# Performance work log

Hardware: AMD Instinct MI355X
Metric: run time of the kernel (lower is better)

The kernel has to match this reference:

```python
import jax, jax.numpy as jnp
import numpy as np

B, S, D = 2, 2048, 1024
H = 16
DH = D // H


def _layernorm(x, g, b, eps=1e-5):
    mu = jnp.mean(x, axis=-1, keepdims=True)
    var = jnp.var(x, axis=-1, keepdims=True)
    return (x - mu) * jax.lax.rsqrt(var + eps) * g + b


def setup_inputs() -> dict:
    key = jax.random.key(0)
    ks = jax.random.split(key, 8)
    s = lambda fan_in: 1.0 / np.sqrt(fan_in)
    return {
        "x": jax.random.normal(ks[0], (B, S, D), dtype=jnp.float32),
        "ln1_g": jnp.ones((D,), jnp.float32),
        "ln1_b": jnp.zeros((D,), jnp.float32),
        "w_qkv": jax.random.uniform(ks[1], (D, 3 * D), jnp.float32, -s(D), s(D)),
        "b_qkv": jnp.zeros((3 * D,), jnp.float32),
        "w_out": jax.random.uniform(ks[2], (D, D), jnp.float32, -s(D), s(D)),
        "b_out": jnp.zeros((D,), jnp.float32),
        "ln2_g": jnp.ones((D,), jnp.float32),
        "ln2_b": jnp.zeros((D,), jnp.float32),
        "w1": jax.random.uniform(ks[3], (D, 4 * D), jnp.float32, -s(D), s(D)),
        "b1": jnp.zeros((4 * D,), jnp.float32),
        "w2": jax.random.uniform(ks[4], (4 * D, D), jnp.float32, -s(4 * D), s(4 * D)),
        "b2": jnp.zeros((D,), jnp.float32),
    }


def reference(x, ln1_g, ln1_b, w_qkv, b_qkv, w_out, b_out,
              ln2_g, ln2_b, w1, b1, w2, b2):
    scale = DH ** -0.5
    residual = x
    h = _layernorm(x, ln1_g, ln1_b)
    qkv = h @ w_qkv + b_qkv                      # [B,S,3D]
    q, k, v = jnp.split(qkv, 3, axis=-1)
    # [B,S,D] -> [B,H,S,DH]
    split_heads = lambda t: t.reshape(B, S, H, DH).transpose(0, 2, 1, 3)
    q, k, v = map(split_heads, (q, k, v))
    scores = jnp.einsum("bhsd,bhtd->bhst", q, k) * scale  # full O(S^2) matrix
    attn = jax.nn.softmax(scores, axis=-1)
    out = jnp.einsum("bhst,bhtd->bhsd", attn, v)
    out = out.transpose(0, 2, 1, 3).reshape(B, S, D)
    out = out @ w_out + b_out                    # dropout is identity at eval
    x = residual + out
    residual = x
    h = _layernorm(x, ln2_g, ln2_b)
    h = jax.nn.gelu(h @ w1 + b1, approximate=False)
    h = h @ w2 + b2
    return residual + h
```

## Files before the change

### kernel.cpp

```cpp
#include <hip/hip_runtime.h>
#include <hip/hip_bf16.h>
#include <math.h>

#define Bc 2
#define Sc 2048
#define Dc 1024
#define Hc 16
#define DHc 64
#define Mc (Bc*Sc)

typedef __attribute__((ext_vector_type(8))) short bf16x8;
typedef __attribute__((ext_vector_type(4))) float f32x4;
typedef __attribute__((ext_vector_type(16))) float f32x16;

#define QSCALE 0.18033688f

__device__ __forceinline__ ushort f2bf(float f){
  union { float f; uint32_t u; } c; c.f = f;
  uint32_t u = c.u;
  return (ushort)((u + 0x7fffu + ((u >> 16) & 1u)) >> 16);
}
__device__ __forceinline__ ushort f2bf_fast(float f){
  union { float f; uint32_t u; } c; c.f = f;
  return (ushort)((c.u + 0x8000u) >> 16);
}
__device__ __forceinline__ float fast_exp2(float x){
#if __has_builtin(__builtin_amdgcn_exp2f)
  return __builtin_amdgcn_exp2f(x);
#else
  return exp2f(x);
#endif
}

__device__ __forceinline__ void stage16(const void* g, void* lbase, int lane){
#if __has_builtin(__builtin_amdgcn_global_load_lds)
  __builtin_amdgcn_global_load_lds(
      (const __attribute__((address_space(1))) void*)g,
      (__attribute__((address_space(3))) void*)lbase, 16, 0, 0);
#else
  *(int4*)((char*)lbase + lane*16) = *(const int4*)g;
#endif
}

__global__ __launch_bounds__(256) void tcast(const float* __restrict__ w,
                                             ushort* __restrict__ wt,
                                             int K, int N){
  __shared__ float t[32][33];
  int kb = blockIdx.y * 32, nb = blockIdx.x * 32;
  int tx = threadIdx.x & 31, ty = threadIdx.x >> 5;
  #pragma unroll
  for (int i = 0; i < 4; i++)
    t[ty + 8*i][tx] = w[(size_t)(kb + ty + 8*i) * N + nb + tx];
  __syncthreads();
  #pragma unroll
  for (int i = 0; i < 4; i++)
    wt[(size_t)(nb + ty + 8*i) * K + kb + tx] = f2bf(t[tx][ty + 8*i]);
}

__global__ __launch_bounds__(256) void ln_bf16(const float* __restrict__ x,
                                               const float* __restrict__ g,
                                               const float* __restrict__ b,
                                               ushort* __restrict__ out){
  int row = blockIdx.x;
  const float4 xv = reinterpret_cast<const float4*>(x + (size_t)row * Dc)[threadIdx.x];
  float s  = xv.x + xv.y + xv.z + xv.w;
  float sq = xv.x*xv.x + xv.y*xv.y + xv.z*xv.z + xv.w*xv.w;
  #pragma unroll
  for (int m = 1; m < 64; m <<= 1){ s += __shfl_xor(s, m); sq += __shfl_xor(sq, m); }
  __shared__ float ss[4], ssq[4];
  int wv = threadIdx.x >> 6;
  if ((threadIdx.x & 63) == 0){ ss[wv] = s; ssq[wv] = sq; }
  __syncthreads();
  s  = ss[0] + ss[1] + ss[2] + ss[3];
  sq = ssq[0] + ssq[1] + ssq[2] + ssq[3];
  float mu  = s * (1.0f / Dc);
  float var = sq * (1.0f / Dc) - mu * mu;
  float rstd = rsqrtf(var + 1e-5f);
  float4 gv = reinterpret_cast<const float4*>(g)[threadIdx.x];
  float4 bv = reinterpret_cast<const float4*>(b)[threadIdx.x];
  ushort o[4];
  o[0] = f2bf((xv.x - mu) * rstd * gv.x + bv.x);
  o[1] = f2bf((xv.y - mu) * rstd * gv.y + bv.y);
  o[2] = f2bf((xv.z - mu) * rstd * gv.z + bv.z);
  o[3] = f2bf((xv.w - mu) * rstd * gv.w + bv.w);
  *reinterpret_cast<uint2*>(out + (size_t)row * Dc + threadIdx.x * 4) =
      *reinterpret_cast<uint2*>(o);
}

template<int EPI>
__global__ __launch_bounds__(256) void gemm128(
    const ushort* __restrict__ A, const ushort* __restrict__ BT,
    const float* __restrict__ bias,
    ushort* __restrict__ outb,
    ushort* __restrict__ oq, ushort* __restrict__ ok, ushort* __restrict__ ov,
    int N, int K){
  __shared__ short As[2][128*32];
  __shared__ short Bs[2][128*32];

  const int fid = blockIdx.x;
  const int q8 = gridDim.x >> 3;
  const int id2 = (fid & 7) * q8 + (fid >> 3);
  const int nbx = N / 128;
  const int nb = id2 % nbx, mb = id2 / nbx;

  const int tid = threadIdx.x;
  const int wave = tid >> 6, lane = tid & 63;
  const int wm = wave >> 1, wn = wave & 1;
  const int lr = lane & 15, lg = lane >> 4;

  f32x4 acc[4][4] = {};

  const int sr = tid >> 2;
  const int sc = ((tid & 3) * 8) ^ ((sr & 3) * 8);
  const ushort* Ag = A  + (size_t)(mb * 128 + sr) * K + sc;
  const ushort* Bg = BT + (size_t)(nb * 128 + sr) * K + sc;
  const int nK = K >> 5;

  {
    char* Ab = (char*)&As[0][0] + wave * 1024;
    char* Bb = (char*)&Bs[0][0] + wave * 1024;
    stage16(Ag,                 Ab,        lane);
    stage16(Ag + (size_t)64*K,  Ab + 4096, lane);
    stage16(Bg,                 Bb,        lane);
    stage16(Bg + (size_t)64*K,  Bb + 4096, lane);
  }
  __syncthreads();

  const int rsz = (lr & 3) * 8;

  for (int kt = 0; kt < nK; ++kt){
    const int cur = kt & 1;
    if (kt + 1 < nK){
      const int ko = (kt + 1) * 32;
      char* Ab = (char*)&As[cur ^ 1][0] + wave * 1024;
      char* Bb = (char*)&Bs[cur ^ 1][0] + wave * 1024;
      stage16(Ag + ko,                 Ab,        lane);
      stage16(Ag + (size_t)64*K + ko,  Ab + 4096, lane);
      stage16(Bg + ko,                 Bb,        lane);
      stage16(Bg + (size_t)64*K + ko,  Bb + 4096, lane);
    }
    bf16x8 af[4], bfr[4];
    #pragma unroll
    for (int mt = 0; mt < 4; mt++)
      af[mt] = *reinterpret_cast<const bf16x8*>(
          &As[cur][(wm*64 + mt*16 + lr)*32 + ((lg*8) ^ rsz)]);
    #pragma unroll
    for (int nt = 0; nt < 4; nt++)
      bfr[nt] = *reinterpret_cast<const bf16x8*>(
          &Bs[cur][(wn*64 + nt*16 + lr)*32 + ((lg*8) ^ rsz)]);
    #pragma unroll
    for (int mt = 0; mt < 4; mt++)
      #pragma unroll
      for (int nt = 0; nt < 4; nt++)
        acc[mt][nt] = __builtin_amdgcn_mfma_f32_16x16x32_bf16(af[mt], bfr[nt], acc[mt][nt], 0, 0, 0);
    __syncthreads();
  }

  if (EPI == 0){
    #pragma unroll
    for (int mt = 0; mt < 4; mt++){
      const int gm0 = mb * 128 + wm * 64 + mt * 16 + lg * 4;
      const int bb = gm0 >> 11, s0 = gm0 & 2047;
      #pragma unroll
      for (int nt = 0; nt < 4; nt++){
        const int gn = nb * 128 + wn * 64 + nt * 16 + lr;
        const float bv = bias[gn];
        const int p = gn >> 10, d = gn & 1023;
        const int hh = d >> 6, dh = d & 63;
        const int bh = bb * Hc + hh;
        if (p == 2){
          ushort pk[4];
          #pragma unroll
          for (int r = 0; r < 4; r++) pk[r] = f2bf(acc[mt][nt][r] + bv);
          *reinterpret_cast<uint2*>(ov + ((size_t)bh * DHc + dh) * Sc + s0) =
              *reinterpret_cast<uint2*>(pk);
        } else if (p == 0){
          #pragma unroll
          for (int r = 0; r < 4; r++)
            oq[((size_t)bh * Sc + s0 + r) * DHc + dh] = f2bf((acc[mt][nt][r] + bv) * QSCALE);
        } else {
          #pragma unroll
          for (int r = 0; r < 4; r++)
            ok[((size_t)bh * Sc + s0 + r) * DHc + dh] = f2bf(acc[mt][nt][r] + bv);
        }
      }
    }
  } else {
    #pragma unroll
    for (int mt = 0; mt < 4; mt++){
      #pragma unroll
      for (int nt = 0; nt < 4; nt++){
        #pragma unroll
        for (int r = 0; r < 4; r++){
          const int gm = mb * 128 + wm * 64 + mt * 16 + lg * 4 + r;
          const int gn = nb * 128 + wn * 64 + nt * 16 + lr;
          float val = acc[mt][nt][r] + bias[gn];
          float ge = 0.5f * val * (1.0f + erff(val * 0.70710678118f));
          outb[(size_t)gm * N + gn] = f2bf(ge);
        }
      }
    }
  }
}

__global__ __launch_bounds__(256) void gemm64_32(
    const ushort* __restrict__ A, const ushort* __restrict__ BT,
    const float* __restrict__ bias, const float* __restrict__ res,
    float* __restrict__ outf, int N, int K){
  __shared__ short As[2][128*32];
  __shared__ short Bs[2][64*32];

  const int fid = blockIdx.x;
  const int q8 = gridDim.x >> 3;
  const int id2 = (fid & 7) * q8 + (fid >> 3);
  const int nbx = N / 64;
  const int nb = id2 % nbx, mb = id2 / nbx;

  const int tid = threadIdx.x;
  const int wave = tid >> 6, lane = tid & 63;
  const int wm = wave >> 1, wn = wave & 1;
  const int l31 = lane & 31, lg2 = lane >> 5;

  f32x16 acc0 = {}, acc1 = {};

  const int sr = tid >> 2;
  const int sc = ((tid & 3) * 8) ^ ((sr & 3) * 8);
  const ushort* Ag = A  + (size_t)(mb * 128 + sr) * K + sc;
  const ushort* Bg = BT + (size_t)(nb * 64  + sr) * K + sc;
  const int nK = K >> 5;

  {
    char* Ab = (char*)&As[0][0] + wave * 1024;
    char* Bb = (char*)&Bs[0][0] + wave * 1024;
    stage16(Ag,                Ab,        lane);
    stage16(Ag + (size_t)64*K, Ab + 4096, lane);
    stage16(Bg,                Bb,        lane);
  }
  __syncthreads();

  const int rx = (l31 & 3) * 8;
  const int c0 = (lg2 * 8) ^ rx;
  const int c1 = (16 + lg2 * 8) ^ rx;

  for (int kt = 0; kt < nK; ++kt){
    const int cur = kt & 1;
    if (kt + 1 < nK){
      const int ko = (kt + 1) * 32;
      char* Ab = (char*)&As[cur ^ 1][0] + wave * 1024;
      char* Bb = (char*)&Bs[cur ^ 1][0] + wave * 1024;
      stage16(Ag + ko,                Ab,        lane);
      stage16(Ag + (size_t)64*K + ko, Ab + 4096, lane);
      stage16(Bg + ko,                Bb,        lane);
    }
    bf16x8 a00 = *reinterpret_cast<const bf16x8*>(&As[cur][(wm*64 +      l31)*32 + c0]);
    bf16x8 a01 = *reinterpret_cast<const bf16x8*>(&As[cur][(wm*64 +      l31)*32 + c1]);
    bf16x8 a10 = *reinterpret_cast<const bf16x8*>(&As[cur][(wm*64 + 32 + l31)*32 + c0]);
    bf16x8 a11 = *reinterpret_cast<const bf16x8*>(&As[cur][(wm*64 + 32 + l31)*32 + c1]);
    bf16x8 b0  = *reinterpret_cast<const bf16x8*>(&Bs[cur][(wn*32 + l31)*32 + c0]);
    bf16x8 b1  = *reinterpret_cast<const bf16x8*>(&Bs[cur][(wn*32 + l31)*32 + c1]);
    acc0 = __builtin_amdgcn_mfma_f32_32x32x16_bf16(a00, b0, acc0, 0, 0, 0);
    acc0 = __builtin_amdgcn_mfma_f32_32x32x16_bf16(a01, b1, acc0, 0, 0, 0);
    acc1 = __builtin_amdgcn_mfma_f32_32x32x16_bf16(a10, b0, acc1, 0, 0, 0);
    acc1 = __builtin_amdgcn_mfma_f32_32x32x16_bf16(a11, b1, acc1, 0, 0, 0);
    __syncthreads();
  }

  const int gn = nb * 64 + wn * 32 + l31;
  const float bv = bias[gn];
  #pragma unroll
  for (int r = 0; r < 16; r++){
    const int rl = (r & 3) + 8 * (r >> 2) + 4 * lg2;
    {
      const int gm = mb * 128 + wm * 64 + rl;
      const size_t i = (size_t)gm * N + gn;
      outf[i] = acc0[r] + bv + res[i];
    }
    {
      const int gm = mb * 128 + wm * 64 + 32 + rl;
      const size_t i = (size_t)gm * N + gn;
      outf[i] = acc1[r] + bv + res[i];
    }
  }
}

__global__ __launch_bounds__(256) void flash_attn(const ushort* __restrict__ q,
                                                  const ushort* __restrict__ k,
                                                  const ushort* __restrict__ vt,
                                                  ushort* __restrict__ ctx){
  const int bh = blockIdx.y;
  const int q0 = blockIdx.x * 64;
  const int b  = bh >> 4, h = bh & 15;
  const int tid = threadIdx.x, wave = tid >> 6, lane = tid & 63;
  const int lr = lane & 15, lg = lane >> 4;

  __shared__ short Kt[2][64*64];
  __shared__ short Vt[64*64];
  __shared__ short Ps[4][16][68];

  const int g8  = lane & 7;
  const int kr0 = wave * 8 + (lane >> 3);
  const int kcol = (g8 ^ (kr0 & 7)) * 8;
  const ushort* kg0 = k + (size_t)bh * Sc * DHc + (size_t)kr0 * DHc + kcol;
  const ushort* kg1 = kg0 + 32 * DHc;
  char* Kl = (char*)&Kt[0][0] + wave * 1024;
  const int KBUFB = 64 * 64 * 2;

  const int vrow = tid >> 3, vg8 = tid & 7;
  const int vcol = (vg8 ^ (vrow & 7)) * 8;
  const ushort* vg0 = vt + (size_t)bh * DHc * Sc + (size_t)vrow * Sc + vcol;
  const ushort* vg1 = vg0 + (size_t)32 * Sc;

  bf16x8 qf0, qf1;
  {
    const ushort* qp = q + (size_t)bh * Sc * DHc + (size_t)(q0 + wave * 16 + lr) * DHc + lg * 8;
    qf0 = *reinterpret_cast<const bf16x8*>(qp);
    qf1 = *reinterpret_cast<const bf16x8*>(qp + 32);
  }

  f32x4 o[4] = {};
  float lp[4] = {0.f, 0.f, 0.f, 0.f};
  constexpr int NTILES = Sc / 64;

  stage16(kg0, Kl,        lane);
  stage16(kg1, Kl + 4096, lane);
  {
    int4 w0 = *reinterpret_cast<const int4*>(vg0);
    int4 w1 = *reinterpret_cast<const int4*>(vg1);
    *reinterpret_cast<int4*>((char*)&Vt[0] + tid * 16)        = w0;
    *reinterpret_cast<int4*>((char*)&Vt[0] + 4096 + tid * 16) = w1;
  }
  __syncthreads();

  const int swz = (lr & 7) * 8;

  for (int kt = 0; kt < NTILES; ++kt){
    const int cur = kt & 1;
    int4 vr0, vr1;
    if (kt + 1 < NTILES){
      const int nx = (cur ^ 1) * KBUFB;
      stage16(kg0 + (size_t)(kt + 1) * 64 * DHc, Kl + nx,        lane);
      stage16(kg1 + (size_t)(kt + 1) * 64 * DHc, Kl + nx + 4096, lane);
      vr0 = *reinterpret_cast<const int4*>(vg0 + (kt + 1) * 64);
      vr1 = *reinterpret_cast<const int4*>(vg1 + (kt + 1) * 64);
    }

    f32x4 sacc[4];
    __builtin_amdgcn_s_setprio(1);
    #pragma unroll
    for (int nt = 0; nt < 4; nt++){
      const int rb = (nt * 16 + lr) * 64;
      bf16x8 b0 = *reinterpret_cast<const bf16x8*>(&Kt[cur][rb + ((lg * 8) ^ swz)]);
      bf16x8 b1 = *reinterpret_cast<const bf16x8*>(&Kt[cur][rb + ((32 + lg * 8) ^ swz)]);
      f32x4 z = {0.f, 0.f, 0.f, 0.f};
      z = __builtin_amdgcn_mfma_f32_16x16x32_bf16(qf0, b0, z, 0, 0, 0);
      z = __builtin_amdgcn_mfma_f32_16x16x32_bf16(qf1, b1, z, 0, 0, 0);
      sacc[nt] = z;
    }
    __builtin_amdgcn_s_setprio(0);

    #pragma unroll
    for (int nt = 0; nt < 4; nt++){
      #pragma unroll
      for (int j = 0; j < 4; j++){
        float p = fast_exp2(sacc[nt][j]);
        lp[j] += p;
        Ps[wave][lg * 4 + j][nt * 16 + lr] = (short)f2bf_fast(p);
      }
    }

    bf16x8 pf0 = *reinterpret_cast<const bf16x8*>(&Ps[wave][lr][lg * 8]);
    bf16x8 pf1 = *reinterpret_cast<const bf16x8*>(&Ps[wave][lr][32 + lg * 8]);
    __builtin_amdgcn_s_setprio(1);
    #pragma unroll
    for (int nt = 0; nt < 4; nt++){
      const int rb = (nt * 16 + lr) * 64;
      bf16x8 v0 = *reinterpret_cast<const bf16x8*>(&Vt[rb + ((lg * 8) ^ swz)]);
      bf16x8 v1 = *reinterpret_cast<const bf16x8*>(&Vt[rb + ((32 + lg * 8) ^ swz)]);
      o[nt] = __builtin_amdgcn_mfma_f32_16x16x32_bf16(pf0, v0, o[nt], 0, 0, 0);
      o[nt] = __builtin_amdgcn_mfma_f32_16x16x32_bf16(pf1, v1, o[nt], 0, 0, 0);
    }
    __builtin_amdgcn_s_setprio(0);

    __syncthreads();
    if (kt + 1 < NTILES){
      *reinterpret_cast<int4*>((char*)&Vt[0] + tid * 16)        = vr0;
      *reinterpret_cast<int4*>((char*)&Vt[0] + 4096 + tid * 16) = vr1;
      __syncthreads();
    }
  }

  #pragma unroll
  for (int m = 1; m < 16; m <<= 1)
    #pragma unroll
    for (int j = 0; j < 4; j++) lp[j] += __shfl_xor(lp[j], m);

  #pragma unroll
  for (int j = 0; j < 4; j++){
    float inv = 1.0f / lp[j];
    int s = q0 + wave * 16 + lg * 4 + j;
    ushort* op = ctx + ((size_t)b * Sc + s) * Dc + h * DHc;
    #pragma unroll
    for (int nt = 0; nt < 4; nt++)
      op[nt * 16 + lr] = f2bf(o[nt][j] * inv);
  }
}

extern "C" void kernel_launch(void* const* d_in, const int* in_sizes, int n_in,
                              void* d_out, int out_size, void* d_ws, size_t ws_size,
                              hipStream_t stream){
  const float* x     = (const float*)d_in[0];
  const float* ln1_g = (const float*)d_in[1];
  const float* ln1_b = (const float*)d_in[2];
  const float* w_qkv = (const float*)d_in[3];
  const float* b_qkv = (const float*)d_in[4];
  const float* w_out = (const float*)d_in[5];
  const float* b_out = (const float*)d_in[6];
  const float* ln2_g = (const float*)d_in[7];
  const float* ln2_b = (const float*)d_in[8];
  const float* w1    = (const float*)d_in[9];
  const float* b1    = (const float*)d_in[10];
  const float* w2    = (const float*)d_in[11];
  const float* b2    = (const float*)d_in[12];
  float* out = (float*)d_out;

  char* ws = (char*)d_ws;
  size_t off = 0;
  ushort* wqkvT = (ushort*)(ws + off); off += (size_t)3072 * 1024 * 2;
  ushort* woutT = (ushort*)(ws + off); off += (size_t)1024 * 1024 * 2;
  ushort* w1T   = (ushort*)(ws + off); off += (size_t)4096 * 1024 * 2;
  ushort* w2T   = (ushort*)(ws + off); off += (size_t)1024 * 4096 * 2;
  ushort* hln   = (ushort*)(ws + off); off += (size_t)Mc * Dc * 2;
  ushort* qbuf  = (ushort*)(ws + off); off += (size_t)32 * Sc * DHc * 2;
  ushort* kbuf  = (ushort*)(ws + off); off += (size_t)32 * Sc * DHc * 2;
  ushort* vtbuf = (ushort*)(ws + off); off += (size_t)32 * Sc * DHc * 2;
  ushort* ctx   = (ushort*)(ws + off); off += (size_t)Mc * Dc * 2;
  float*  x1    = (float*)(ws + off);  off += (size_t)Mc * Dc * 4;
  ushort* act   = qbuf;

  tcast<<<dim3(3072 / 32, 1024 / 32), 256, 0, stream>>>(w_qkv, wqkvT, 1024, 3072);
  tcast<<<dim3(1024 / 32, 1024 / 32), 256, 0, stream>>>(w_out, woutT, 1024, 1024);
  tcast<<<dim3(4096 / 32, 1024 / 32), 256, 0, stream>>>(w1,    w1T,   1024, 4096);
  tcast<<<dim3(1024 / 32, 4096 / 32), 256, 0, stream>>>(w2,    w2T,   4096, 1024);

  ln_bf16<<<Mc, 256, 0, stream>>>(x, ln1_g, ln1_b, hln);

  gemm128<0><<<(3072/128) * (Mc/128), 256, 0, stream>>>(
      hln, wqkvT, b_qkv, nullptr, qbuf, kbuf, vtbuf, 3072, 1024);

  flash_attn<<<dim3(Sc / 64, 32), 256, 0, stream>>>(qbuf, kbuf, vtbuf, ctx);

  gemm64_32<<<(1024/64) * (Mc/128), 256, 0, stream>>>(
      ctx, woutT, b_out, x, x1, 1024, 1024);

  ln_bf16<<<Mc, 256, 0, stream>>>(x1, ln2_g, ln2_b, hln);

  gemm128<2><<<(4096/128) * (Mc/128), 256, 0, stream>>>(
      hln, w1T, b1, act, nullptr, nullptr, nullptr, 4096, 1024);

  gemm64_32<<<(1024/64) * (Mc/128), 256, 0, stream>>>(
      act, w2T, b2, x1, out, 1024, 4096);
}
```

Measured before the change: 291.8 us.

## Switch residual GEMM to 16x16 MFMA and transpose attention score tile

The residual-output GEMM (out-proj and FFN2) moves from two 32x32x16 MFMA accumulators to eight 16x16x32 MFMA tiles per wave, with matching LDS fragment loads and epilogue indexing. In flash attention the QK^T MFMA operands are swapped so each lane holds four consecutive keys for one query. P can then be packed with a hardware v_cvt_pk_bf16_f32 and written as one 8-byte LDS store instead of four scalar stores. The row-sum becomes a single scalar per lane reduced with two shuffles. These changes add more MFMA issues in the GEMM and inline asm that depends on the target ISA.

```diff
diff --git a/kernel.cpp b/kernel.cpp
--- a/kernel.cpp
+++ b/kernel.cpp
@@ -11,7 +11,6 @@
 
 typedef __attribute__((ext_vector_type(8))) short bf16x8;
 typedef __attribute__((ext_vector_type(4))) float f32x4;
-typedef __attribute__((ext_vector_type(16))) float f32x16;
 
 #define QSCALE 0.18033688f
 
@@ -19,10 +18,6 @@
   union { float f; uint32_t u; } c; c.f = f;
   uint32_t u = c.u;
   return (ushort)((u + 0x7fffu + ((u >> 16) & 1u)) >> 16);
-}
-__device__ __forceinline__ ushort f2bf_fast(float f){
-  union { float f; uint32_t u; } c; c.f = f;
-  return (ushort)((c.u + 0x8000u) >> 16);
 }
 __device__ __forceinline__ float fast_exp2(float x){
 #if __has_builtin(__builtin_amdgcn_exp2f)
@@ -30,6 +25,11 @@
 #else
   return exp2f(x);
 #endif
+}
+__device__ __forceinline__ uint32_t cvt_pk_bf16(float a, float b){
+  uint32_t r;
+  asm("v_cvt_pk_bf16_f32 %0, %1, %2" : "=v"(r) : "v"(a), "v"(b));
+  return r;
 }
 
 __device__ __forceinline__ void stage16(const void* g, void* lbase, int lane){
@@ -203,7 +203,7 @@
   }
 }
 
-__global__ __launch_bounds__(256) void gemm64_32(
+__global__ __launch_bounds__(256) void gemm_res64(
     const ushort* __restrict__ A, const ushort* __restrict__ BT,
     const float* __restrict__ bias, const float* __restrict__ res,
     float* __restrict__ outf, int N, int K){
@@ -219,9 +219,9 @@
   const int tid = threadIdx.x;
   const int wave = tid >> 6, lane = tid & 63;
   const int wm = wave >> 1, wn = wave & 1;
-  const int l31 = lane & 31, lg2 = lane >> 5;
-
-  f32x16 acc0 = {}, acc1 = {};
+  const int lr = lane & 15, lg = lane >> 4;
+
+  f32x4 acc[4][2] = {};
 
   const int sr = tid >> 2;
   const int sc = ((tid & 3) * 8) ^ ((sr & 3) * 8);
@@ -238,9 +238,7 @@
   }
   __syncthreads();
 
-  const int rx = (l31 & 3) * 8;
-  const int c0 = (lg2 * 8) ^ rx;
-  const int c1 = (16 + lg2 * 8) ^ rx;
+  const int rsz = (lr & 3) * 8;
 
   for (int kt = 0; kt < nK; ++kt){
     const int cur = kt & 1;
@@ -252,33 +250,34 @@
       stage16(Ag + (size_t)64*K + ko, Ab + 4096, lane);
       stage16(Bg + ko,                Bb,        lane);
     }
-    bf16x8 a00 = *reinterpret_cast<const bf16x8*>(&As[cur][(wm*64 +      l31)*32 + c0]);
-    bf16x8 a01 = *reinterpret_cast<const bf16x8*>(&As[cur][(wm*64 +      l31)*32 + c1]);
-    bf16x8 a10 = *reinterpret_cast<const bf16x8*>(&As[cur][(wm*64 + 32 + l31)*32 + c0]);
-    bf16x8 a11 = *reinterpret_cast<const bf16x8*>(&As[cur][(wm*64 + 32 + l31)*32 + c1]);
-    bf16x8 b0  = *reinterpret_cast<const bf16x8*>(&Bs[cur][(wn*32 + l31)*32 + c0]);
-    bf16x8 b1  = *reinterpret_cast<const bf16x8*>(&Bs[cur][(wn*32 + l31)*32 + c1]);
-    acc0 = __builtin_amdgcn_mfma_f32_32x32x16_bf16(a00, b0, acc0, 0, 0, 0);
-    acc0 = __builtin_amdgcn_mfma_f32_32x32x16_bf16(a01, b1, acc0, 0, 0, 0);
-    acc1 = __builtin_amdgcn_mfma_f32_32x32x16_bf16(a10, b0, acc1, 0, 0, 0);
-    acc1 = __builtin_amdgcn_mfma_f32_32x32x16_bf16(a11, b1, acc1, 0, 0, 0);
+    bf16x8 af[4], bfr[2];
+    #pragma unroll
+    for (int mt = 0; mt < 4; mt++)
+      af[mt] = *reinterpret_cast<const bf16x8*>(
+          &As[cur][(wm*64 + mt*16 + lr)*32 + ((lg*8) ^ rsz)]);
+    #pragma unroll
+    for (int nt = 0; nt < 2; nt++)
+      bfr[nt] = *reinterpret_cast<const bf16x8*>(
+          &Bs[cur][(wn*32 + nt*16 + lr)*32 + ((lg*8) ^ rsz)]);
+    #pragma unroll
+    for (int mt = 0; mt < 4; mt++)
+      #pragma unroll
+      for (int nt = 0; nt < 2; nt++)
+        acc[mt][nt] = __builtin_amdgcn_mfma_f32_16x16x32_bf16(af[mt], bfr[nt], acc[mt][nt], 0, 0, 0);
     __syncthreads();
   }
 
-  const int gn = nb * 64 + wn * 32 + l31;
-  const float bv = bias[gn];
   #pragma unroll
-  for (int r = 0; r < 16; r++){
-    const int rl = (r & 3) + 8 * (r >> 2) + 4 * lg2;
-    {
-      const int gm = mb * 128 + wm * 64 + rl;
-      const size_t i = (size_t)gm * N + gn;
-      outf[i] = acc0[r] + bv + res[i];
-    }
-    {
-      const int gm = mb * 128 + wm * 64 + 32 + rl;
-      const size_t i = (size_t)gm * N + gn;
-      outf[i] = acc1[r] + bv + res[i];
+  for (int mt = 0; mt < 4; mt++){
+    #pragma unroll
+    for (int nt = 0; nt < 2; nt++){
+      #pragma unroll
+      for (int r = 0; r < 4; r++){
+        const int gm = mb * 128 + wm * 64 + mt * 16 + lg * 4 + r;
+        const int gn = nb * 64 + wn * 32 + nt * 16 + lr;
+        const size_t i = (size_t)gm * N + gn;
+        outf[i] = acc[mt][nt][r] + bias[gn] + res[i];
+      }
     }
   }
 }
@@ -318,7 +317,7 @@
   }
 
   f32x4 o[4] = {};
-  float lp[4] = {0.f, 0.f, 0.f, 0.f};
+  float lps = 0.f;
   constexpr int NTILES = Sc / 64;
 
   stage16(kg0, Kl,        lane);
@@ -352,20 +351,23 @@
       bf16x8 b0 = *reinterpret_cast<const bf16x8*>(&Kt[cur][rb + ((lg * 8) ^ swz)]);
       bf16x8 b1 = *reinterpret_cast<const bf16x8*>(&Kt[cur][rb + ((32 + lg * 8) ^ swz)]);
       f32x4 z = {0.f, 0.f, 0.f, 0.f};
-      z = __builtin_amdgcn_mfma_f32_16x16x32_bf16(qf0, b0, z, 0, 0, 0);
-      z = __builtin_amdgcn_mfma_f32_16x16x32_bf16(qf1, b1, z, 0, 0, 0);
+      z = __builtin_amdgcn_mfma_f32_16x16x32_bf16(b0, qf0, z, 0, 0, 0);
+      z = __builtin_amdgcn_mfma_f32_16x16x32_bf16(b1, qf1, z, 0, 0, 0);
       sacc[nt] = z;
     }
     __builtin_amdgcn_s_setprio(0);
 
     #pragma unroll
     for (int nt = 0; nt < 4; nt++){
-      #pragma unroll
-      for (int j = 0; j < 4; j++){
-        float p = fast_exp2(sacc[nt][j]);
-        lp[j] += p;
-        Ps[wave][lg * 4 + j][nt * 16 + lr] = (short)f2bf_fast(p);
-      }
+      float p0 = fast_exp2(sacc[nt][0]);
+      float p1 = fast_exp2(sacc[nt][1]);
+      float p2 = fast_exp2(sacc[nt][2]);
+      float p3 = fast_exp2(sacc[nt][3]);
+      lps += (p0 + p1) + (p2 + p3);
+      uint2 wd;
+      wd.x = cvt_pk_bf16(p0, p1);
+      wd.y = cvt_pk_bf16(p2, p3);
+      *reinterpret_cast<uint2*>(&Ps[wave][lr][nt * 16 + lg * 4]) = wd;
     }
 
     bf16x8 pf0 = *reinterpret_cast<const bf16x8*>(&Ps[wave][lr][lg * 8]);
@@ -389,14 +391,12 @@
     }
   }
 
-  #pragma unroll
-  for (int m = 1; m < 16; m <<= 1)
-    #pragma unroll
-    for (int j = 0; j < 4; j++) lp[j] += __shfl_xor(lp[j], m);
+  lps += __shfl_xor(lps, 16);
+  lps += __shfl_xor(lps, 32);
 
   #pragma unroll
   for (int j = 0; j < 4; j++){
-    float inv = 1.0f / lp[j];
+    float inv = 1.0f / __shfl(lps, lg * 4 + j);
     int s = q0 + wave * 16 + lg * 4 + j;
     ushort* op = ctx + ((size_t)b * Sc + s) * Dc + h * DHc;
     #pragma unroll
@@ -449,7 +449,7 @@
 
   flash_attn<<<dim3(Sc / 64, 32), 256, 0, stream>>>(qbuf, kbuf, vtbuf, ctx);
 
-  gemm64_32<<<(1024/64) * (Mc/128), 256, 0, stream>>>(
+  gemm_res64<<<(1024/64) * (Mc/128), 256, 0, stream>>>(
       ctx, woutT, b_out, x, x1, 1024, 1024);
 
   ln_bf16<<<Mc, 256, 0, stream>>>(x1, ln2_g, ln2_b, hln);
@@ -457,6 +457,6 @@
   gemm128<2><<<(4096/128) * (Mc/128), 256, 0, stream>>>(
       hln, w1T, b1, act, nullptr, nullptr, nullptr, 4096, 1024);
 
-  gemm64_32<<<(1024/64) * (Mc/128), 256, 0, stream>>>(
+  gemm_res64<<<(1024/64) * (Mc/128), 256, 0, stream>>>(
       act, w2T, b2, x1, out, 1024, 4096);
 }
```

Result: faster. 274.5 us (-5.9%).
